# Kernel optimization log

Measured on AMD Instinct MI355X. Metric: run time of the kernel, lower is better.

## Reference

```python
import jax, jax.numpy as jnp
import numpy as np

EMBED = 768
HEADS = 12
MLP_DIM = 3072
EPS = 1e-5


def _layernorm(x, g, b):
    mu = jnp.mean(x, axis=-1, keepdims=True)
    var = jnp.mean(jnp.square(x - mu), axis=-1, keepdims=True)
    return (x - mu) * jax.lax.rsqrt(var + EPS) * g + b


def setup_inputs() -> dict:
    key = jax.random.key(0)
    ks = jax.random.split(key, 8)
    B, N, C, M = 4, 1024, EMBED, MLP_DIM
    # xavier-ish scales
    x = jax.random.normal(ks[0], (B, N, C), dtype=jnp.float32)
    w_qkv = jax.random.normal(ks[1], (C, 3 * C), dtype=jnp.float32) * (2.0 / (C + 3 * C)) ** 0.5
    w_out = jax.random.normal(ks[2], (C, C), dtype=jnp.float32) * (1.0 / C) ** 0.5
    b_out = jnp.zeros((C,), dtype=jnp.float32)
    ln1_g = jnp.ones((C,), dtype=jnp.float32)
    ln1_b = jnp.zeros((C,), dtype=jnp.float32)
    ln2_g = jnp.ones((C,), dtype=jnp.float32)
    ln2_b = jnp.zeros((C,), dtype=jnp.float32)
    w1 = jax.random.normal(ks[3], (C, M), dtype=jnp.float32) * (2.0 / (C + M)) ** 0.5
    b1 = jnp.zeros((M,), dtype=jnp.float32)
    w2 = jax.random.normal(ks[4], (M, C), dtype=jnp.float32) * (2.0 / (C + M)) ** 0.5
    b2 = jnp.zeros((C,), dtype=jnp.float32)
    return {"x": x, "ln1_g": ln1_g, "ln1_b": ln1_b, "w_qkv": w_qkv, "w_out": w_out,
            "b_out": b_out, "ln2_g": ln2_g, "ln2_b": ln2_b, "w1": w1, "b1": b1,
            "w2": w2, "b2": b2}


def _block(x, ln1_g, ln1_b, w_qkv, w_out, b_out, ln2_g, ln2_b, w1, b1, w2, b2):
    B, N, C = x.shape
    H = HEADS
    D = C // H
    # ---- attention sub-block (note: original Attention adds its own residual
    # on the *normalized* input, and EncoderBlock adds x again) ----
    h = _layernorm(x, ln1_g, ln1_b)
    qkv = (h @ w_qkv).reshape(B, N, 3, H, D)
    q = qkv[:, :, 0].transpose(0, 2, 1, 3)  # [B,H,N,D]
    k = qkv[:, :, 1].transpose(0, 2, 1, 3)
    v = qkv[:, :, 2].transpose(0, 2, 1, 3)
    scores = jnp.einsum('bhnd,bhmd->bhnm', q, k) / jnp.sqrt(jnp.float32(D))
    probs = jax.nn.softmax(scores, axis=-1)
    attn = jnp.einsum('bhnm,bhmd->bhnd', probs, v)
    attn = attn.transpose(0, 2, 1, 3).reshape(B, N, C)
    attn = attn @ w_out + b_out
    x = x + (h + attn)  # double residual, faithful to source
    # ---- MLP sub-block ----
    h2 = _layernorm(x, ln2_g, ln2_b)
    h2 = jax.nn.gelu(h2 @ w1 + b1, approximate=False)
    h2 = h2 @ w2 + b2
    return x + h2


def reference(x, ln1_g, ln1_b, w_qkv, w_out, b_out, ln2_g, ln2_b, w1, b1, w2, b2):
    return _block(x, ln1_g, ln1_b, w_qkv, w_out, b_out, ln2_g, ln2_b, w1, b1, w2, b2)
```

## Files before the change

kernel.cpp:

```cpp
#include <hip/hip_runtime.h>

#define EMBED 768
#define HEADS 12
#define HDIM 64
#define MLP_DIM 3072
#define BATCH 4
#define SEQ 1024
#define ROWS (BATCH*SEQ)
#define LN_EPS 1e-5f

typedef __bf16 bf16x8 __attribute__((ext_vector_type(8)));
typedef float f32x4 __attribute__((ext_vector_type(4)));

__device__ __forceinline__ float bf2f(unsigned short h) {
    unsigned u = ((unsigned)h) << 16;
    return __builtin_bit_cast(float, u);
}
__device__ __forceinline__ unsigned short f2bf(float f) {
    unsigned u = __builtin_bit_cast(unsigned, f);
    unsigned r = (u + 0x7fffu + ((u >> 16) & 1u)) >> 16;
    return (unsigned short)r;
}

__device__ __forceinline__ void async_load16(const unsigned short* g, unsigned short* l) {
    __builtin_amdgcn_global_load_lds(
        (const __attribute__((address_space(1))) unsigned int*)g,
        (__attribute__((address_space(3))) unsigned int*)l,
        16, 0, 0);
}

__global__ void sort_vecs(const float* a0, const float* a1, const float* a2,
                          const float* a3, const float* a4, const float* a5,
                          float* g1, float* be1, float* bo,
                          float* g2, float* be2, float* bb2)
{
    const float* src[6] = {a0, a1, a2, a3, a4, a5};
    float* gdst[2] = {g1, g2};
    float* bdst[4] = {be1, bo, be2, bb2};
    float* dst[6];
    int gi = 0, bi = 0;
    for (int t = 0; t < 6; t++) {
        bool ones = (src[t][0] == 1.0f);
        if (ones) dst[t] = (gi < 2) ? gdst[gi++] : bdst[bi++];
        else      dst[t] = (bi < 4) ? bdst[bi++] : gdst[gi++];
    }
    int t = threadIdx.x;
    for (int k = 0; k < 6; k++) dst[k][t] = src[k][t];
}

__global__ void transpose_weights(const float* __restrict__ wqkv,
                                  const float* __restrict__ wout,
                                  const float* __restrict__ w1,
                                  const float* __restrict__ w2,
                                  unsigned short* __restrict__ wqkvT,
                                  unsigned short* __restrict__ woutT,
                                  unsigned short* __restrict__ w1T,
                                  unsigned short* __restrict__ w2T)
{
    __shared__ unsigned short t[32][33];
    int fb = blockIdx.x;
    const float* src; unsigned short* dst; int gx, ild, old;
    if (fb < 1728)      { src = wqkv; dst = wqkvT; gx = 72; ild = 2304; old = 768; }
    else if (fb < 2304) { fb -= 1728; src = wout; dst = woutT; gx = 24; ild = 768;  old = 768; }
    else if (fb < 4608) { fb -= 2304; src = w1;   dst = w1T;   gx = 96; ild = 3072; old = 768; }
    else                { fb -= 4608; src = w2;   dst = w2T;   gx = 24; ild = 768;  old = 3072; }
    const int j0 = (fb % gx) * 32, i0 = (fb / gx) * 32;
#pragma unroll
    for (int r = 0; r < 4; r++)
        t[threadIdx.y + r*8][threadIdx.x] =
            f2bf(src[(long)(i0 + threadIdx.y + r*8) * ild + (j0 + threadIdx.x)]);
    __syncthreads();
#pragma unroll
    for (int r = 0; r < 4; r++)
        dst[(long)(j0 + threadIdx.y + r*8) * old + (i0 + threadIdx.x)] =
            t[threadIdx.x][threadIdx.y + r*8];
}

__global__ void transpose_any(const void* __restrict__ in,
                              unsigned short* __restrict__ out,
                              int ild, int old,
                              long in_zo, long in_zi, long out_zo, long out_zi,
                              int zdiv, int in_is_f32)
{
    __shared__ unsigned short t[32][33];
    const int z = blockIdx.z;
    const long ib = (long)(z / zdiv) * in_zo  + (long)(z % zdiv) * in_zi;
    const long ob = (long)(z / zdiv) * out_zo + (long)(z % zdiv) * out_zi;
    const int j0 = blockIdx.x * 32, i0 = blockIdx.y * 32;
#pragma unroll
    for (int r = 0; r < 4; r++) {
        long idx = ib + (long)(i0 + threadIdx.y + r*8) * ild + (j0 + threadIdx.x);
        t[threadIdx.y + r*8][threadIdx.x] =
            in_is_f32 ? f2bf(((const float*)in)[idx]) : ((const unsigned short*)in)[idx];
    }
    __syncthreads();
#pragma unroll
    for (int r = 0; r < 4; r++)
        out[ob + (long)(j0 + threadIdx.y + r*8) * old + (i0 + threadIdx.x)] =
            t[threadIdx.x][threadIdx.y + r*8];
}

__global__ void ln_kernel(const float* __restrict__ xin,
                          const float* __restrict__ g,
                          const float* __restrict__ b,
                          unsigned short* __restrict__ out)
{
    const int row = blockIdx.x;
    const int tid = threadIdx.x;
    const long base = (long)row * EMBED;
    float v[3];
#pragma unroll
    for (int i = 0; i < 3; i++) v[i] = xin[base + tid + i * 256];
    float s = v[0] + v[1] + v[2];
    float s2 = v[0]*v[0] + v[1]*v[1] + v[2]*v[2];
    for (int off = 32; off; off >>= 1) { s += __shfl_down(s, off); s2 += __shfl_down(s2, off); }
    __shared__ float ps[4], ps2[4];
    int w = tid >> 6, l = tid & 63;
    if (l == 0) { ps[w] = s; ps2[w] = s2; }
    __syncthreads();
    float ts  = ps[0] + ps[1] + ps[2] + ps[3];
    float ts2 = ps2[0] + ps2[1] + ps2[2] + ps2[3];
    float mu = ts * (1.0f / EMBED);
    float var = ts2 * (1.0f / EMBED) - mu * mu;
    float rs = rsqrtf(var + LN_EPS);
#pragma unroll
    for (int i = 0; i < 3; i++) {
        int c = tid + i * 256;
        out[base + c] = f2bf((v[i] - mu) * rs * g[c] + b[c]);
    }
}

__global__ __launch_bounds__(256) void flash_attn(
    const unsigned short* __restrict__ qkv,
    const unsigned short* __restrict__ vT,
    unsigned short* __restrict__ attn)
{
    __shared__ __align__(16) unsigned short QPs[64 * 64];
    __shared__ __align__(16) unsigned short Ks[2][64 * 64];
    __shared__ __align__(16) unsigned short Vs[2][64 * 64];

    const int tid = threadIdx.x;
    const int wave = tid >> 6, lane = tid & 63;
    const int quad = lane >> 4, lr = lane & 15;
    const int q0 = blockIdx.x * 64;
    const int bh = blockIdx.y;
    const int b = bh / HEADS, h = bh % HEADS;

    const unsigned short* qb = qkv + (size_t)b * SEQ * 3 * EMBED + h * HDIM;
    const unsigned short* kb = qb + EMBED;
    const unsigned short* vb = vT + (size_t)bh * HDIM * SEQ;

#pragma unroll
    for (int cb = 0; cb < 512; cb += 256) {
        int p = cb + tid, r = p >> 3, cc = (p & 7) ^ (r & 7);
        async_load16(qb + (long)(q0 + r) * (3 * EMBED) + cc * 8, QPs + p * 8);
        async_load16(kb + (long)r * (3 * EMBED) + cc * 8, Ks[0] + p * 8);
        async_load16(vb + (long)r * SEQ + cc * 8, Vs[0] + p * 8);
    }
    __syncthreads();

    bf16x8 aq[2];
#pragma unroll
    for (int s = 0; s < 2; s++) {
        int row = wave * 16 + lr;
        aq[s] = *(const bf16x8*)&QPs[(row * 8 + ((s * 4 + quad) ^ (row & 7))) * 8];
    }

    f32x4 oacc[4];
#pragma unroll
    for (int j = 0; j < 4; j++) oacc[j] = (f32x4){0.f, 0.f, 0.f, 0.f};
    float lpart[4] = {0.f, 0.f, 0.f, 0.f};

    int cur = 0;
    for (int t = 0; t < SEQ / 64; t++) {
        bool pf = (t + 1 < SEQ / 64);
        if (pf) {
            int kv0 = (t + 1) * 64;
#pragma unroll
            for (int cb = 0; cb < 512; cb += 256) {
                int p = cb + tid, r = p >> 3, cc = (p & 7) ^ (r & 7);
                async_load16(kb + (long)(kv0 + r) * (3 * EMBED) + cc * 8, Ks[cur ^ 1] + p * 8);
                async_load16(vb + (long)r * SEQ + kv0 + cc * 8, Vs[cur ^ 1] + p * 8);
            }
        }
        f32x4 sacc[4];
#pragma unroll
        for (int j = 0; j < 4; j++) sacc[j] = (f32x4){0.f, 0.f, 0.f, 0.f};
#pragma unroll
        for (int s = 0; s < 2; s++)
#pragma unroll
            for (int j = 0; j < 4; j++) {
                int row = j * 16 + lr;
                bf16x8 bk = *(const bf16x8*)&Ks[cur][(row * 8 + ((s * 4 + quad) ^ (lr & 7))) * 8];
                sacc[j] = __builtin_amdgcn_mfma_f32_16x16x32_bf16(aq[s], bk, sacc[j], 0, 0, 0);
            }
#pragma unroll
        for (int j = 0; j < 4; j++)
#pragma unroll
            for (int r = 0; r < 4; r++) {
                float e = __expf(sacc[j][r] * 0.125f);
                lpart[r] += e;
                int row = wave * 16 + quad * 4 + r;
                int cc = (2 * j + (lr >> 3)) ^ (row & 7);
                QPs[(row * 8 + cc) * 8 + (lr & 7)] = f2bf(e);
            }
#pragma unroll
        for (int s = 0; s < 2; s++) {
            int prow = wave * 16 + lr;
            bf16x8 ap = *(const bf16x8*)&QPs[(prow * 8 + ((s * 4 + quad) ^ (prow & 7))) * 8];
#pragma unroll
            for (int j = 0; j < 4; j++) {
                int vrow = j * 16 + lr;
                bf16x8 bv = *(const bf16x8*)&Vs[cur][(vrow * 8 + ((s * 4 + quad) ^ (lr & 7))) * 8];
                oacc[j] = __builtin_amdgcn_mfma_f32_16x16x32_bf16(ap, bv, oacc[j], 0, 0, 0);
            }
        }
        __syncthreads();
        cur ^= 1;
    }
#pragma unroll
    for (int off = 1; off < 16; off <<= 1)
#pragma unroll
        for (int r = 0; r < 4; r++) lpart[r] += __shfl_xor(lpart[r], off);
#pragma unroll
    for (int j = 0; j < 4; j++)
#pragma unroll
        for (int r = 0; r < 4; r++) {
            int row = q0 + wave * 16 + quad * 4 + r;
            attn[(size_t)(b * SEQ + row) * EMBED + h * HDIM + j * 16 + lr] =
                f2bf(oacc[j][r] / lpart[r]);
        }
}

__global__ __launch_bounds__(256) void gemm_bt0(
    const unsigned short* __restrict__ A, int lda,
    const unsigned short* __restrict__ Bt, int ldb,
    int Kdim,
    const float* __restrict__ bias,
    unsigned short* __restrict__ Cb,
    int ldc, int gelu_flag)
{
    constexpr int BK = 64;
    __shared__ __align__(16) unsigned short As[128 * BK];
    __shared__ __align__(16) unsigned short Bs[128 * BK];

    const int tid = threadIdx.x;
    const int wave = tid >> 6;
    const int lane = tid & 63;

    int bx = blockIdx.x, by = blockIdx.y;
    {
        int flat = by * gridDim.x + bx;
        int xcd = flat & 7, seq = flat >> 3;
        int ypg = gridDim.y >> 3;
        by = xcd * ypg + seq / gridDim.x;
        bx = seq % gridDim.x;
    }
    const int m0 = by * 128;
    const int n0 = bx * 128;
    const int wrow = (wave >> 1) * 64;
    const int wcol = (wave & 1) * 64;

    f32x4 acc[4][4];
#pragma unroll
    for (int i = 0; i < 4; i++)
#pragma unroll
        for (int j = 0; j < 4; j++) acc[i][j] = (f32x4){0.f, 0.f, 0.f, 0.f};

    const int quad = lane >> 4;
    const int lrow = lane & 15;

    for (int k0 = 0; k0 < Kdim; k0 += BK) {
#pragma unroll
        for (int cb = 0; cb < 4; cb++) {
            int q = cb * 256 + tid;
            int r = q >> 3, c = (q & 7) * 8;
            async_load16(A  + (long)(m0 + r) * lda + k0 + c, As + q * 8);
            async_load16(Bt + (long)(n0 + r) * ldb + k0 + c, Bs + q * 8);
        }
        __syncthreads();

#pragma unroll
        for (int s = 0; s < 2; s++) {
            bf16x8 af[4], bfv[4];
#pragma unroll
            for (int i = 0; i < 4; i++)
                af[i] = *reinterpret_cast<const bf16x8*>(
                    &As[(wrow + i*16 + lrow) * BK + s*32 + quad*8]);
#pragma unroll
            for (int j = 0; j < 4; j++)
                bfv[j] = *reinterpret_cast<const bf16x8*>(
                    &Bs[(wcol + j*16 + lrow) * BK + s*32 + quad*8]);
#pragma unroll
            for (int i = 0; i < 4; i++)
#pragma unroll
                for (int j = 0; j < 4; j++)
                    acc[i][j] = __builtin_amdgcn_mfma_f32_16x16x32_bf16(
                        af[i], bfv[j], acc[i][j], 0, 0, 0);
        }
        __syncthreads();
    }

#pragma unroll
    for (int i = 0; i < 4; i++)
#pragma unroll
        for (int j = 0; j < 4; j++)
#pragma unroll
            for (int r = 0; r < 4; r++) {
                int row = m0 + wrow + i*16 + quad*4 + r;
                int col = n0 + wcol + j*16 + lrow;
                float v = acc[i][j][r];
                if (bias) v += bias[col];
                if (gelu_flag) v = 0.5f * v * (1.0f + erff(v * 0.70710678118654752f));
                Cb[(long)row * ldc + col] = f2bf(v);
            }
}

__global__ __launch_bounds__(256) void gemm_bt64(
    const unsigned short* __restrict__ A, int lda,
    const unsigned short* __restrict__ Bt, int ldb,
    int Kdim,
    const float* __restrict__ bias,
    const unsigned short* __restrict__ res1,
    const float* __restrict__ resf,
    float* __restrict__ Cf,
    unsigned short* __restrict__ Cb,
    int ldc)
{
    __shared__ __align__(16) unsigned short As[2][64 * 64];
    __shared__ __align__(16) unsigned short Bs[2][64 * 64];

    const int tid = threadIdx.x;
    const int wave = tid >> 6;
    const int lane = tid & 63;
    const int quad = lane >> 4;
    const int lr = lane & 15;

    int bx = blockIdx.x, by = blockIdx.y;
    {
        int flat = by * gridDim.x + bx;
        int xcd = flat & 7, seq = flat >> 3;
        int ypg = gridDim.y >> 3;
        by = xcd * ypg + seq / gridDim.x;
        bx = seq % gridDim.x;
    }
    const int m0 = by * 64;
    const int n0 = bx * 64;

    f32x4 acc[4];
#pragma unroll
    for (int j = 0; j < 4; j++) acc[j] = (f32x4){0.f, 0.f, 0.f, 0.f};

    auto stage = [&](int k0, unsigned short* Ad, unsigned short* Bd) {
#pragma unroll
        for (int cb = 0; cb < 512; cb += 256) {
            int p = cb + tid, r = p >> 3, cc = (p & 7) ^ (r & 7);
            async_load16(A + (long)(m0 + r) * lda + k0 + cc * 8, Ad + p * 8);
            async_load16(Bt + (long)(n0 + r) * ldb + k0 + cc * 8, Bd + p * 8);
        }
    };

    stage(0, As[0], Bs[0]);
    __syncthreads();
    int cur = 0;

    for (int k0 = 0; k0 < Kdim; k0 += 64) {
        if (k0 + 64 < Kdim) stage(k0 + 64, As[cur ^ 1], Bs[cur ^ 1]);

#pragma unroll
        for (int s = 0; s < 2; s++) {
            int arow = wave * 16 + lr;
            bf16x8 af = *(const bf16x8*)&As[cur][(arow * 8 + ((s * 4 + quad) ^ (lr & 7))) * 8];
#pragma unroll
            for (int j = 0; j < 4; j++) {
                int brow = j * 16 + lr;
                bf16x8 bv = *(const bf16x8*)&Bs[cur][(brow * 8 + ((s * 4 + quad) ^ (lr & 7))) * 8];
                acc[j] = __builtin_amdgcn_mfma_f32_16x16x32_bf16(af, bv, acc[j], 0, 0, 0);
            }
        }
        __syncthreads();
        cur ^= 1;
    }

#pragma unroll
    for (int j = 0; j < 4; j++)
#pragma unroll
        for (int r = 0; r < 4; r++) {
            int row = m0 + wave * 16 + quad * 4 + r;
            int col = n0 + j * 16 + lr;
            float v = acc[j][r];
            if (bias) v += bias[col];
            long idx = (long)row * ldc + col;
            if (res1) v += bf2f(res1[idx]);
            if (resf) v += resf[idx];
            if (Cf) Cf[idx] = v;
            else    Cb[idx] = f2bf(v);
        }
}

extern "C" void kernel_launch(void* const* d_in, const int* in_sizes, int n_in,
                              void* d_out, int out_size, void* d_ws, size_t ws_size,
                              hipStream_t stream)
{
    int ix = -1, iwqkv = -1, iwout = -1, iw1 = -1, iw2 = -1, ib1 = -1;
    int v768[8]; int nv = 0;
    for (int i = 0; i < n_in; i++) {
        int s = in_sizes[i];
        if      (s == ROWS*EMBED)        ix = i;
        else if (s == EMBED*3*EMBED)     iwqkv = i;
        else if (s == EMBED*EMBED)       iwout = i;
        else if (s == EMBED*MLP_DIM)     { if (iw1 < 0) iw1 = i; else iw2 = i; }
        else if (s == MLP_DIM)           ib1 = i;
        else if (s == EMBED && nv < 8)   v768[nv++] = i;
    }
    if (n_in != 12 || ix < 0 || iwqkv < 0 || iwout < 0 || iw1 < 0 || iw2 < 0 ||
        ib1 < 0 || nv != 6)
        return;

    const float* x    = (const float*)d_in[ix];
    const float* wqkv = (const float*)d_in[iwqkv];
    const float* wout = (const float*)d_in[iwout];
    const float* w1   = (const float*)d_in[iw1];
    const float* w2   = (const float*)d_in[iw2];
    const float* b1   = (const float*)d_in[ib1];
    float* out = (float*)d_out;

    char* ws = (char*)d_ws;
    size_t off = 0;
    auto alloc = [&](size_t bytes) -> char* {
        char* p = ws + off;
        off += (bytes + 255) & ~(size_t)255;
        return p;
    };
    unsigned short* h_bf  = (unsigned short*)alloc((size_t)ROWS * EMBED * 2);
    unsigned short* qkv   = (unsigned short*)alloc((size_t)ROWS * 3 * EMBED * 2);
    unsigned short* vT    = (unsigned short*)alloc((size_t)BATCH * HEADS * HDIM * SEQ * 2);
    unsigned short* attn  = (unsigned short*)alloc((size_t)ROWS * EMBED * 2);
    float*          x2f   = (float*)alloc((size_t)ROWS * EMBED * 4);
    unsigned short* wqkvT = (unsigned short*)alloc((size_t)3 * EMBED * EMBED * 2);
    unsigned short* woutT = (unsigned short*)alloc((size_t)EMBED * EMBED * 2);
    unsigned short* w1T   = (unsigned short*)alloc((size_t)MLP_DIM * EMBED * 2);
    unsigned short* w2T   = (unsigned short*)alloc((size_t)EMBED * MLP_DIM * 2);
    unsigned short* h2    = (unsigned short*)alloc((size_t)ROWS * EMBED * 2);
    float* vecs           = (float*)alloc((size_t)(6 * EMBED) * 4);
    if (off > ws_size) return;

    float* ln1g_f = vecs;
    float* ln1b_f = vecs + EMBED;
    float* bout_f = vecs + 2 * EMBED;
    float* ln2g_f = vecs + 3 * EMBED;
    float* ln2b_f = vecs + 4 * EMBED;
    float* b2_f   = vecs + 5 * EMBED;
    unsigned short* u = qkv;

    sort_vecs<<<1, 768, 0, stream>>>(
        (const float*)d_in[v768[0]], (const float*)d_in[v768[1]],
        (const float*)d_in[v768[2]], (const float*)d_in[v768[3]],
        (const float*)d_in[v768[4]], (const float*)d_in[v768[5]],
        ln1g_f, ln1b_f, bout_f, ln2g_f, ln2b_f, b2_f);

    dim3 tb(32, 8);
    transpose_weights<<<6912, tb, 0, stream>>>(wqkv, wout, w1, w2,
                                               wqkvT, woutT, w1T, w2T);

    ln_kernel<<<ROWS, 256, 0, stream>>>(x, ln1g_f, ln1b_f, h_bf);

    gemm_bt0<<<dim3(3*EMBED/128, ROWS/128), 256, 0, stream>>>(
        h_bf, EMBED, wqkvT, EMBED, EMBED, nullptr, qkv, 3*EMBED, 0);

    transpose_any<<<dim3(HDIM/32, SEQ/32, BATCH*HEADS), tb, 0, stream>>>(
        qkv + 2*EMBED, vT, 3*EMBED, SEQ,
        (long)SEQ*3*EMBED, (long)HDIM,
        (long)HEADS*HDIM*SEQ, (long)HDIM*SEQ, HEADS, 0);

    flash_attn<<<dim3(SEQ/64, BATCH*HEADS), 256, 0, stream>>>(qkv, vT, attn);

    gemm_bt64<<<dim3(EMBED/64, ROWS/64), 256, 0, stream>>>(
        attn, EMBED, woutT, EMBED, EMBED,
        bout_f, h_bf, x, x2f, nullptr, EMBED);

    ln_kernel<<<ROWS, 256, 0, stream>>>(x2f, ln2g_f, ln2b_f, h2);

    gemm_bt0<<<dim3(MLP_DIM/128, ROWS/128), 256, 0, stream>>>(
        h2, EMBED, w1T, EMBED, EMBED, b1, u, MLP_DIM, 1);

    gemm_bt64<<<dim3(EMBED/64, ROWS/64), 256, 0, stream>>>(
        u, MLP_DIM, w2T, MLP_DIM, MLP_DIM,
        b2_f, nullptr, x2f, out, nullptr, EMBED);
}
```

Before: 328.3 us.

## Double-buffer gemm_bt0 LDS tiles and use 512 threads with smaller BK

Restructures the 128x128 GEMM used for the QKV and first MLP projections. It uses 8 waves instead of 4, each owning a 64x32 sub-tile. BK drops to 32 and the A/B tiles are double-buffered, so the next K slice is fetched asynchronously while MFMAs run on the current one. The aim is to hide global-to-LDS latency and raise occupancy. In exchange there are twice as many K iterations and barriers, and each wave does less MFMA work per barrier.

```diff
diff --git a/kernel.cpp b/kernel.cpp
--- a/kernel.cpp
+++ b/kernel.cpp
@@ -232,7 +232,7 @@
         }
 }
 
-__global__ __launch_bounds__(256) void gemm_bt0(
+__global__ __launch_bounds__(512) void gemm_bt0(
     const unsigned short* __restrict__ A, int lda,
     const unsigned short* __restrict__ Bt, int ldb,
     int Kdim,
@@ -240,13 +240,17 @@
     unsigned short* __restrict__ Cb,
     int ldc, int gelu_flag)
 {
-    constexpr int BK = 64;
-    __shared__ __align__(16) unsigned short As[128 * BK];
-    __shared__ __align__(16) unsigned short Bs[128 * BK];
+    constexpr int BK = 32;
+    __shared__ __align__(16) unsigned short As[2][128 * BK];
+    __shared__ __align__(16) unsigned short Bs[2][128 * BK];
 
     const int tid = threadIdx.x;
     const int wave = tid >> 6;
     const int lane = tid & 63;
+    const int quad = lane >> 4;
+    const int lrow = lane & 15;
+    const int wr = wave >> 2;
+    const int wc = wave & 3;
 
     int bx = blockIdx.x, by = blockIdx.y;
     {
@@ -258,57 +262,58 @@
     }
     const int m0 = by * 128;
     const int n0 = bx * 128;
-    const int wrow = (wave >> 1) * 64;
-    const int wcol = (wave & 1) * 64;
-
-    f32x4 acc[4][4];
+
+    f32x4 acc[4][2];
 #pragma unroll
     for (int i = 0; i < 4; i++)
 #pragma unroll
-        for (int j = 0; j < 4; j++) acc[i][j] = (f32x4){0.f, 0.f, 0.f, 0.f};
-
-    const int quad = lane >> 4;
-    const int lrow = lane & 15;
+        for (int j = 0; j < 2; j++) acc[i][j] = (f32x4){0.f, 0.f, 0.f, 0.f};
+
+    const int srow = tid >> 2;
+    const int scol = (tid & 3) * 8;
+
+    auto stage = [&](int k0, int bsel) {
+        async_load16(A  + (long)(m0 + srow) * lda + k0 + scol,
+                     (unsigned short*)As[bsel] + tid * 8);
+        async_load16(Bt + (long)(n0 + srow) * ldb + k0 + scol,
+                     (unsigned short*)Bs[bsel] + tid * 8);
+    };
+
+    stage(0, 0);
+    __syncthreads();
+    int cur = 0;
 
     for (int k0 = 0; k0 < Kdim; k0 += BK) {
-#pragma unroll
-        for (int cb = 0; cb < 4; cb++) {
-            int q = cb * 256 + tid;
-            int r = q >> 3, c = (q & 7) * 8;
-            async_load16(A  + (long)(m0 + r) * lda + k0 + c, As + q * 8);
-            async_load16(Bt + (long)(n0 + r) * ldb + k0 + c, Bs + q * 8);
-        }
+        if (k0 + BK < Kdim) stage(k0 + BK, cur ^ 1);
+
+        bf16x8 af[4], bfv[2];
+#pragma unroll
+        for (int i = 0; i < 4; i++)
+            af[i] = *reinterpret_cast<const bf16x8*>(
+                &As[cur][(wr*64 + i*16 + lrow) * BK + quad * 8]);
+#pragma unroll
+        for (int j = 0; j < 2; j++)
+            bfv[j] = *reinterpret_cast<const bf16x8*>(
+                &Bs[cur][(wc*32 + j*16 + lrow) * BK + quad * 8]);
+#pragma unroll
+        for (int i = 0; i < 4; i++)
+#pragma unroll
+            for (int j = 0; j < 2; j++)
+                acc[i][j] = __builtin_amdgcn_mfma_f32_16x16x32_bf16(
+                    af[i], bfv[j], acc[i][j], 0, 0, 0);
+
         __syncthreads();
-
-#pragma unroll
-        for (int s = 0; s < 2; s++) {
-            bf16x8 af[4], bfv[4];
-#pragma unroll
-            for (int i = 0; i < 4; i++)
-                af[i] = *reinterpret_cast<const bf16x8*>(
-                    &As[(wrow + i*16 + lrow) * BK + s*32 + quad*8]);
-#pragma unroll
-            for (int j = 0; j < 4; j++)
-                bfv[j] = *reinterpret_cast<const bf16x8*>(
-                    &Bs[(wcol + j*16 + lrow) * BK + s*32 + quad*8]);
-#pragma unroll
-            for (int i = 0; i < 4; i++)
-#pragma unroll
-                for (int j = 0; j < 4; j++)
-                    acc[i][j] = __builtin_amdgcn_mfma_f32_16x16x32_bf16(
-                        af[i], bfv[j], acc[i][j], 0, 0, 0);
-        }
-        __syncthreads();
+        cur ^= 1;
     }
 
 #pragma unroll
     for (int i = 0; i < 4; i++)
 #pragma unroll
-        for (int j = 0; j < 4; j++)
+        for (int j = 0; j < 2; j++)
 #pragma unroll
             for (int r = 0; r < 4; r++) {
-                int row = m0 + wrow + i*16 + quad*4 + r;
-                int col = n0 + wcol + j*16 + lrow;
+                int row = m0 + wr*64 + i*16 + quad*4 + r;
+                int col = n0 + wc*32 + j*16 + lrow;
                 float v = acc[i][j][r];
                 if (bias) v += bias[col];
                 if (gelu_flag) v = 0.5f * v * (1.0f + erff(v * 0.70710678118654752f));
@@ -465,7 +470,7 @@
 
     ln_kernel<<<ROWS, 256, 0, stream>>>(x, ln1g_f, ln1b_f, h_bf);
 
-    gemm_bt0<<<dim3(3*EMBED/128, ROWS/128), 256, 0, stream>>>(
+    gemm_bt0<<<dim3(3*EMBED/128, ROWS/128), 512, 0, stream>>>(
         h_bf, EMBED, wqkvT, EMBED, EMBED, nullptr, qkv, 3*EMBED, 0);
 
     transpose_any<<<dim3(HDIM/32, SEQ/32, BATCH*HEADS), tb, 0, stream>>>(
@@ -481,7 +486,7 @@
 
     ln_kernel<<<ROWS, 256, 0, stream>>>(x2f, ln2g_f, ln2b_f, h2);
 
-    gemm_bt0<<<dim3(MLP_DIM/128, ROWS/128), 256, 0, stream>>>(
+    gemm_bt0<<<dim3(MLP_DIM/128, ROWS/128), 512, 0, stream>>>(
         h2, EMBED, w1T, EMBED, EMBED, b1, u, MLP_DIM, 1);
 
     gemm_bt64<<<dim3(EMBED/64, ROWS/64), 256, 0, stream>>>(
```

New measurement: 278.2 us. 15.3% less time.
